# Kernel optimization log

Hardware: AMD Instinct MI355X
Metric: run time of the kernel (lower is better)

Reference implementation:

```python
import jax, jax.numpy as jnp
import numpy as np

N, F1, F2, D = 114, 32, 10, 100
F = F1 + F2
B = 16
EPS = 1e-5


def setup_inputs() -> dict:
    key = jax.random.key(0)
    ks = jax.random.split(key, 20)
    inp = {
        'XE_subs': jax.random.normal(ks[0], (B, 2, N, N, F), jnp.float32),
        'X_subs': jax.random.normal(ks[1], (B, 2, N, F1), jnp.float32),
        'A_subs': (jax.random.uniform(ks[2], (B, 2, N, N)) < 0.15).astype(jnp.float32),
        'XE_pros': jax.random.normal(ks[3], (B, 2, N, N, F), jnp.float32),
        'X_pros': jax.random.normal(ks[4], (B, 2, N, F1), jnp.float32),
        'A_pros': (jax.random.uniform(ks[5], (B, 2, N, N)) < 0.15).astype(jnp.float32),
        'Wi_sub': jax.random.normal(ks[6], (F, D)) * 0.1,
        'Wm1_sub': jax.random.normal(ks[7], (D, D)) * 0.1,
        'Wm2_sub': jax.random.normal(ks[8], (D, D)) * 0.1,
        'Wa_sub': jax.random.normal(ks[9], (D + F1, D)) * 0.1,
        'bn1s_g': jnp.ones((D,)), 'bn1s_b': jnp.zeros((D,)),
        'bn2s_g': jnp.ones((D,)), 'bn2s_b': jnp.zeros((D,)),
        'Wi_pro': jax.random.normal(ks[10], (F, D)) * 0.1,
        'Wm1_pro': jax.random.normal(ks[11], (D, D)) * 0.1,
        'Wm2_pro': jax.random.normal(ks[12], (D, D)) * 0.1,
        'Wa_pro': jax.random.normal(ks[13], (D + F1, D)) * 0.1,
        'bn1p_g': jnp.ones((D,)), 'bn1p_b': jnp.zeros((D,)),
        'bn2p_g': jnp.ones((D,)), 'bn2p_b': jnp.zeros((D,)),
        'bn3_g': jnp.ones((2 * D,)), 'bn3_b': jnp.zeros((2 * D,)),
        'W1': jax.random.normal(ks[14], (2 * D, 32)) * 0.07,
        'b1': jnp.zeros((32,)),
        'W2': jax.random.normal(ks[15], (32, 1)) * 0.17,
        'b2': jnp.zeros((1,)),
        'no_subs': 2, 'no_pros': 2,
    }
    return inp


def _bn4(x, g, b):
    # BatchNorm2d (training stats) over channel = last axis of [B,N,N,D]
    m = jnp.mean(x, axis=(0, 1, 2))
    v = jnp.var(x, axis=(0, 1, 2))
    return (x - m) * (g * jax.lax.rsqrt(v + EPS)) + b


def _branch(XE, X, A, no, Wi, Wm1, Wm2, Wa, g1, b1, g2, b2):
    h_max = None
    for i in range(no):
        xe = XE[:, i]                      # [B,N,N,F]
        a = A[:, i][..., None]             # [B,N,N,1]
        x = X[:, i][:, :, None, :]         # [B,N,1,F1]
        H0 = jax.nn.relu(jnp.einsum('bijf,fd->bijd', xe, Wi))  # [B,N,N,D]

        def mp(H):
            # Ones[N,N] @ transpose(H*A,1,2): column sum of (H*A) over axis 1,
            # broadcast, minus H^T, re-masked by A.
            S = jnp.sum(H * a, axis=1)                          # [B,N,D]
            return (S[:, :, None, :] - jnp.swapaxes(H, 1, 2)) * a

        H1 = jax.nn.relu(_bn4(H0 + jnp.einsum('bijd,de->bije', mp(H0), Wm1), g1, b1))
        H2 = jax.nn.relu(_bn4(H0 + jnp.einsum('bijd,de->bije', mp(H1), Wm2), g2, b2))
        Mv = jnp.sum(H2 * a, axis=2, keepdims=True)             # [B,N,1,D]
        XM = jnp.concatenate([x, Mv], axis=3)                   # [B,N,1,F1+D]
        H = jax.nn.relu(jnp.einsum('bnkf,fd->bnkd', XM, Wa))    # [B,N,1,D]
        h = jnp.sum(H[:, :, 0, :], axis=1)                      # [B,D]  (Ones1_N sum)
        h_max = h if h_max is None else jnp.maximum(h_max, h)
    return h_max


def reference(XE_subs, X_subs, A_subs, XE_pros, X_pros, A_pros,
              Wi_sub, Wm1_sub, Wm2_sub, Wa_sub, bn1s_g, bn1s_b, bn2s_g, bn2s_b,
              Wi_pro, Wm1_pro, Wm2_pro, Wa_pro, bn1p_g, bn1p_b, bn2p_g, bn2p_b,
              bn3_g, bn3_b, W1, b1, W2, b2, no_subs, no_pros):
    h_sub = _branch(XE_subs, X_subs, A_subs, int(no_subs),
                    Wi_sub, Wm1_sub, Wm2_sub, Wa_sub, bn1s_g, bn1s_b, bn2s_g, bn2s_b)
    h_pro = _branch(XE_pros, X_pros, A_pros, int(no_pros),
                    Wi_pro, Wm1_pro, Wm2_pro, Wa_pro, bn1p_g, bn1p_b, bn2p_g, bn2p_b)
    h = jnp.concatenate([h_sub, h_pro], axis=1)                 # [B,2D]
    m = jnp.mean(h, axis=0)
    v = jnp.var(h, axis=0)
    h = (h - m) * (bn3_g * jax.lax.rsqrt(v + EPS)) + bn3_b      # BatchNorm1d
    h = jax.nn.relu(h @ W1 + b1)
    return h @ W2 + b2                                          # [B,1]
```

## Files before the change

kernel.cpp:

```cpp
#include <hip/hip_runtime.h>

#define NN_ 114
#define NSQ (114*114)
#define FF 42
#define F1_ 32
#define DD 100
#define BB 16
#define ROWS (BB*NSQ)
#define NT512 407
#define MAXE 2432
#define NEB (MAXE/64)
#define MAXR 3968
#define EPS 1e-5f

typedef __attribute__((ext_vector_type(8))) short short8;
typedef __attribute__((ext_vector_type(4))) float f32x4;

static __device__ inline short f2bf(float f) {
    unsigned u;
    __builtin_memcpy(&u, &f, 4);
    unsigned r = (u + 0x7FFFu + ((u >> 16) & 1u)) >> 16;
    return (short)r;
}
static __device__ inline float bf2f(short h) {
    unsigned u = ((unsigned)(unsigned short)h) << 16;
    float f;
    __builtin_memcpy(&f, &u, 4);
    return f;
}

__global__ __launch_bounds__(1024) void k_edges(const float* __restrict__ Aa0,
                                                const float* __restrict__ Aa1,
                                                int* __restrict__ Eij, int* __restrict__ Idx,
                                                int* __restrict__ Ridx, int* __restrict__ Rlist,
                                                int* __restrict__ cnt, int* __restrict__ rcnt) {
    int b = blockIdx.x, combo = blockIdx.y;
    int zb = combo*BB + b;
    const float* am = ((combo < 2) ? Aa0 : Aa1) + (long)(b*2 + (combo & 1))*NSQ;
    int tid = threadIdx.x;
    __shared__ unsigned long long m0[NN_], m1[NN_];
    __shared__ int base_e, base_u;
    __shared__ int we[16], wu[16];
    int lane = tid & 63, wv = tid >> 6;
    if (tid == 0) { base_e = 0; base_u = 0; }
    for (int i = wv; i < NN_; i += 16) {
        float v0 = am[i*NN_ + lane];
        unsigned long long w0 = __ballot(v0 != 0.f);
        float v1 = (lane < NN_-64) ? am[i*NN_ + 64 + lane] : 0.f;
        unsigned long long w1 = __ballot(v1 != 0.f);
        if (lane == 0) { m0[i] = w0; m1[i] = w1; }
    }
    __syncthreads();
    for (int c0 = 0; c0 < NSQ; c0 += 1024) {
        int idx = c0 + tid;
        bool pe = false, pu = false;
        if (idx < NSQ) {
            int ii = idx / NN_, jj = idx - ii*NN_;
            pe = (((jj < 64 ? (m0[ii] >> jj) : (m1[ii] >> (jj-64))) & 1ull) != 0);
            bool pt = (((ii < 64 ? (m0[jj] >> ii) : (m1[jj] >> (ii-64))) & 1ull) != 0);
            pu = pe || pt;
        }
        unsigned long long me = __ballot(pe), mu = __ballot(pu);
        if (lane == 0) { we[wv] = __popcll(me); wu[wv] = __popcll(mu); }
        __syncthreads();
        int oe = base_e, ou = base_u;
        for (int w = 0; w < wv; w++) { oe += we[w]; ou += wu[w]; }
        oe += __popcll(me & ((1ull << lane) - 1ull));
        ou += __popcll(mu & ((1ull << lane) - 1ull));
        if (idx < NSQ) {
            bool oke = pe && (oe < MAXE);
            Idx[(long)zb*NSQ + idx]  = oke ? oe : -1;
            if (oke) Eij[zb*MAXE + oe] = idx;
            bool oku = pu && (ou < MAXR);
            Ridx[(long)zb*NSQ + idx] = oku ? ou : -1;
            if (oku) Rlist[(long)zb*MAXR + ou] = idx;
        }
        __syncthreads();
        if (tid == 0) { for (int w = 0; w < 16; w++) { base_e += we[w]; base_u += wu[w]; } }
        __syncthreads();
    }
    if (tid == 0) {
        cnt[zb]  = (base_e < MAXE) ? base_e : MAXE;
        rcnt[zb] = (base_u < MAXR) ? base_u : MAXR;
    }
}

__global__ __launch_bounds__(256) void k_h0stat(const float* __restrict__ XE0,
                                                const float* __restrict__ XE1,
                                                const float* __restrict__ Wi0,
                                                const float* __restrict__ Wi1,
                                                float* __restrict__ P0) {
    __shared__ char smem[16384 + 14336];
    char* Abase = smem;
    char* Bbase = smem + 16384;
    int tid = threadIdx.x;
    int combo = blockIdx.y;
    const float* XE = (combo < 2) ? XE0 : XE1;
    const float* Wi = (combo < 2) ? Wi0 : Wi1;
    int slot = combo & 1;
    for (int c = tid; c < 896; c += 256) {
        int col = c >> 3, k8b = (c & 7) * 8;
        short8 pk;
#pragma unroll
        for (int t = 0; t < 8; t++) {
            int k = k8b + t;
            pk[t] = (col < DD && k < FF) ? f2bf(Wi[k*DD + col]) : (short)0;
        }
        int byte = (col*128 + k8b*2) ^ ((col & 7) << 4);
        *reinterpret_cast<short8*>(Bbase + byte) = pk;
    }
    int w = tid >> 6, l = tid & 63;
    int lr = l & 15, g = l >> 4;
    float psum[7], psq[7];
#pragma unroll
    for (int ct = 0; ct < 7; ct++) { psum[ct] = 0.f; psq[ct] = 0.f; }
    int k8 = (tid & 7) * 8;
    int rbase = tid >> 3;
    for (int sub = 0; sub < 4; sub++) {
        int tileRow = blockIdx.x * 512 + sub * 128;
        float av[4][8];
#pragma unroll
        for (int c4 = 0; c4 < 4; c4++) {
            int r = tileRow + rbase + c4*32;
            if (r < ROWS && k8 < FF) {
                int b = r / NSQ;
                int ij = r - b*NSQ;
                const float* src = XE + ((long)(b*2 + slot)*NSQ + ij)*FF + k8;
                if (k8 <= 32) {
#pragma unroll
                    for (int q = 0; q < 4; q++) {
                        float2 f = *reinterpret_cast<const float2*>(src + q*2);
                        av[c4][q*2] = f.x; av[c4][q*2+1] = f.y;
                    }
                } else {
                    float2 f = *reinterpret_cast<const float2*>(src);
                    av[c4][0] = f.x; av[c4][1] = f.y;
#pragma unroll
                    for (int q = 2; q < 8; q++) av[c4][q] = 0.f;
                }
            } else {
#pragma unroll
                for (int q = 0; q < 8; q++) av[c4][q] = 0.f;
            }
        }
        __syncthreads();
#pragma unroll
        for (int c4 = 0; c4 < 4; c4++) {
            int row = rbase + c4*32;
            short8 pk;
#pragma unroll
            for (int t = 0; t < 8; t++) pk[t] = f2bf(av[c4][t]);
            int byte = (row*128 + k8*2) ^ ((row & 7) << 4);
            *reinterpret_cast<short8*>(Abase + byte) = pk;
        }
        __syncthreads();
        short8 af[2][2];
#pragma unroll
        for (int rt = 0; rt < 2; rt++) {
            int row = (w*2 + rt)*16 + lr;
#pragma unroll
            for (int kf = 0; kf < 2; kf++) {
                int byte = (row*128 + kf*64 + g*16) ^ ((row & 7) << 4);
                af[rt][kf] = *reinterpret_cast<const short8*>(Abase + byte);
            }
        }
#pragma unroll
        for (int ct = 0; ct < 7; ct++) {
            int col = ct*16 + lr;
            int bb0 = (col*128 +  0 + g*16) ^ ((col & 7) << 4);
            int bb1 = (col*128 + 64 + g*16) ^ ((col & 7) << 4);
            short8 bf0 = *reinterpret_cast<const short8*>(Bbase + bb0);
            short8 bf1 = *reinterpret_cast<const short8*>(Bbase + bb1);
            f32x4 a0 = (f32x4){0.f,0.f,0.f,0.f};
            f32x4 a1 = (f32x4){0.f,0.f,0.f,0.f};
            a0 = __builtin_amdgcn_mfma_f32_16x16x32_bf16(af[0][0], bf0, a0, 0, 0, 0);
            a0 = __builtin_amdgcn_mfma_f32_16x16x32_bf16(af[0][1], bf1, a0, 0, 0, 0);
            a1 = __builtin_amdgcn_mfma_f32_16x16x32_bf16(af[1][0], bf0, a1, 0, 0, 0);
            a1 = __builtin_amdgcn_mfma_f32_16x16x32_bf16(af[1][1], bf1, a1, 0, 0, 0);
#pragma unroll
            for (int rr = 0; rr < 4; rr++) {
                float v0 = fmaxf(a0[rr], 0.f);
                float v1 = fmaxf(a1[rr], 0.f);
                psum[ct] += v0 + v1;
                psq[ct]  += v0*v0 + v1*v1;
            }
        }
    }
    __syncthreads();
    float* red_s = (float*)smem;
    float* red_q = red_s + 16*112;
    int idx16 = w*4 + g;
#pragma unroll
    for (int ct = 0; ct < 7; ct++) {
        red_s[idx16*112 + ct*16 + lr] = psum[ct];
        red_q[idx16*112 + ct*16 + lr] = psq[ct];
    }
    __syncthreads();
    if (tid < DD) {
        float s = 0.f, q = 0.f;
#pragma unroll
        for (int t2 = 0; t2 < 16; t2++) { s += red_s[t2*112 + tid]; q += red_q[t2*112 + tid]; }
        P0[((long)combo*NT512 + blockIdx.x)*200 + tid] = s;
        P0[((long)combo*NT512 + blockIdx.x)*200 + 100 + tid] = q;
    }
}

__global__ __launch_bounds__(256) void k_h0u(const float* __restrict__ XE0,
                                             const float* __restrict__ XE1,
                                             const float* __restrict__ Wi0,
                                             const float* __restrict__ Wi1,
                                             const int* __restrict__ Rlist,
                                             const int* __restrict__ rcnt,
                                             float* __restrict__ H0c, int zbase) {
    __shared__ float smem[FF*68 + FF*112];
    float* As = smem;
    float* Bs = smem + FF*68;
    __shared__ int srcOff[64];
    int tid = threadIdx.x;
    int b = blockIdx.y, z = blockIdx.z;
    int combo = zbase + z;
    const float* XE = (combo < 2) ? XE0 : XE1;
    const float* Wi = (combo < 2) ? Wi0 : Wi1;
    int slot = combo & 1;
    int zbE = combo*BB + b;
    int zbH = z*BB + b;
    int rid0 = blockIdx.x * 64;
    int rc = rcnt[zbE];
    if (rid0 >= rc) return;
    if (tid < 64) {
        int rid = rid0 + tid;
        int ij = (rid < rc) ? Rlist[(long)zbE*MAXR + rid] : Rlist[(long)zbE*MAXR];
        srcOff[tid] = ((b*2+slot)*NSQ + ij)*FF;
    }
    for (int idx = tid; idx < FF*112; idx += 256) {
        int kk = idx / 112, col = idx - kk*112;
        Bs[idx] = (col < DD) ? Wi[kk*DD + col] : 0.f;
    }
    __syncthreads();
    for (int idx = tid; idx < 64*FF; idx += 256) {
        int rr = idx / FF, kk = idx - rr*FF;
        As[kk*68 + rr] = XE[(long)srcOff[rr] + kk];
    }
    int ty = tid >> 4, tx = tid & 15;
    float acc[4][7];
#pragma unroll
    for (int i = 0; i < 4; i++)
#pragma unroll
        for (int j = 0; j < 7; j++) acc[i][j] = 0.f;
    __syncthreads();
    for (int kk = 0; kk < FF; kk++) {
        float4 avv = *reinterpret_cast<const float4*>(&As[kk*68 + ty*4]);
#pragma unroll
        for (int cc = 0; cc < 7; cc++) {
            float bv = Bs[kk*112 + tx + 16*cc];
            acc[0][cc] += avv.x*bv; acc[1][cc] += avv.y*bv;
            acc[2][cc] += avv.z*bv; acc[3][cc] += avv.w*bv;
        }
    }
#pragma unroll
    for (int rq = 0; rq < 4; rq++) {
        int rid = rid0 + ty*4 + rq;
        if (rid < rc) {
#pragma unroll
            for (int cc = 0; cc < 7; cc++) {
                int col = tx + 16*cc;
                if (col < DD)
                    H0c[((long)zbH*MAXR + rid)*DD + col] = fmaxf(acc[rq][cc], 0.f);
            }
        }
    }
}

template<int LAYER>
__global__ __launch_bounds__(128) void k_cs(const float* __restrict__ H0c,
                                            const int* __restrict__ Idx,
                                            const int* __restrict__ Ridx,
                                            const float* __restrict__ Dprev,
                                            const float* __restrict__ bnsc,
                                            float* __restrict__ CSp, int zbase) {
    int bi = blockIdx.x, part = blockIdx.y, z = blockIdx.z;
    int b = bi / NN_, i = bi % NN_;
    int zbE = (zbase + z)*BB + b;
    int zbH = z*BB + b;
    int k0 = part*29, k1 = (k0+29 < NN_) ? k0+29 : NN_;
    __shared__ int eid_s[29], row_s[29];
    int tid = threadIdx.x;
    if (tid < k1-k0) {
        long pos = (long)zbE*NSQ + (k0+tid)*NN_ + i;
        eid_s[tid] = Idx[pos];
        row_s[tid] = Ridx[pos];
    }
    __syncthreads();
    if (tid < DD) {
        float sc = 0.f, sh = 0.f;
        if (LAYER == 2) { sc = bnsc[z*200 + tid]; sh = bnsc[z*200 + DD + tid]; }
        float acc = 0.f;
        for (int k = 0; k < k1-k0; k++) {
            int e = eid_s[k];
            if (e >= 0) {
                float v = H0c[((long)zbH*MAXR + row_s[k])*DD + tid];
                if (LAYER == 2) { v += Dprev[((long)zbH*MAXE + e)*DD + tid]; v = fmaxf(v*sc+sh, 0.f); }
                acc += v;
            }
        }
        CSp[(((long)z*BB*NN_ + bi)*4 + part)*DD + tid] = acc;
    }
}

__global__ __launch_bounds__(256) void k_swgemm(const float* __restrict__ CSp,
                                                const float* __restrict__ W0,
                                                const float* __restrict__ W1,
                                                float* __restrict__ SW, int zbase) {
    const int M = BB*NN_;
    __shared__ float smem[50*68 + 50*DD];
    float* As = smem;
    float* Bs = smem + 50*68;
    int tid = threadIdx.x;
    int z = blockIdx.y;
    const float* W = ((zbase + z) < 2) ? W0 : W1;
    const float* In = CSp + (long)z*M*4*DD;
    float* Out = SW + (long)z*M*DD;
    int tileRow = blockIdx.x * 64;
    int ty = tid >> 4, tx = tid & 15;
    float acc[4][7];
#pragma unroll
    for (int i=0;i<4;i++)
#pragma unroll
        for (int j=0;j<7;j++) acc[i][j]=0.f;
    for (int kc = 0; kc < 2; kc++) {
        __syncthreads();
        for (int idx = tid; idx < 64*50; idx += 256) {
            int rr = idx / 50, kk = idx % 50;
            int r = tileRow + rr;
            float v = 0.f;
            if (r < M) {
                long base = (long)r*4*DD + kc*50 + kk;
                v = In[base] + In[base+DD] + In[base+2*DD] + In[base+3*DD];
            }
            As[kk*68 + rr] = v;
        }
        for (int idx = tid; idx < 50*DD; idx += 256) {
            int kk = idx / DD, e = idx % DD;
            Bs[kk*DD + e] = W[(kc*50+kk)*DD + e];
        }
        __syncthreads();
        for (int kk = 0; kk < 50; kk++) {
            float4 av = *reinterpret_cast<const float4*>(&As[kk*68 + ty*4]);
#pragma unroll
            for (int cc=0; cc<7; cc++) {
                int col = tx + 16*cc;
                float bv = (col < DD) ? Bs[kk*DD + col] : 0.f;
                acc[0][cc] += av.x*bv; acc[1][cc] += av.y*bv;
                acc[2][cc] += av.z*bv; acc[3][cc] += av.w*bv;
            }
        }
    }
#pragma unroll
    for (int rq=0;rq<4;rq++){
        int r = tileRow + ty*4 + rq;
        if (r < M) {
#pragma unroll
            for (int cc=0;cc<7;cc++){
                int col = tx+16*cc;
                if (col < DD) Out[(long)r*DD + col] = acc[rq][cc];
            }
        }
    }
}

template<int LAYER>
__global__ __launch_bounds__(256) void k_dcomb(const float* __restrict__ H0c,
                                               const int* __restrict__ Eij,
                                               const int* __restrict__ cnt,
                                               const int* __restrict__ Idx,
                                               const int* __restrict__ Ridx,
                                               const float* __restrict__ Dprev,
                                               const float* __restrict__ Wm0,
                                               const float* __restrict__ Wm1,
                                               const float* __restrict__ SW,
                                               const float* __restrict__ bnsc,
                                               float* __restrict__ Dout,
                                               float* __restrict__ PD, int zbase) {
    __shared__ char smem[45056];
    char* Ahi = smem;
    char* Alo = smem + 8192;
    char* Bhi = smem + 16384;
    char* Blo = smem + 16384 + 14336;
    __shared__ int srcOff[64], addOff[64], h0Off[64], swOff[64];
    __shared__ float s1[DD], t1[DD];
    int tid = threadIdx.x;
    int b = blockIdx.y, z = blockIdx.z;
    int combo = zbase + z;
    const float* Wm = (combo < 2) ? Wm0 : Wm1;
    int zbE = combo*BB + b;
    int zbH = z*BB + b;
    int e0 = blockIdx.x * 64;
    int c = cnt[zbE];
    long pdbase = ((long)zbH*NEB + blockIdx.x)*200;
    if (e0 >= c) {
        if (tid < DD) { PD[pdbase + tid] = 0.f; PD[pdbase + 100 + tid] = 0.f; }
        return;
    }
    if (LAYER == 2 && tid < DD) { s1[tid]=bnsc[z*200+tid]; t1[tid]=bnsc[z*200+DD+tid]; }
    if (tid < 64) {
        int e = e0 + tid;
        if (e < c) {
            int ij = Eij[zbE*MAXE + e];
            int ii = ij / NN_, jj = ij % NN_;
            long tpos = (long)zbE*NSQ + jj*NN_ + ii;
            srcOff[tid] = (zbH*MAXR + Ridx[tpos])*DD;
            h0Off[tid]  = (zbH*MAXR + Ridx[(long)zbE*NSQ + ij])*DD;
            swOff[tid]  = ((z*BB + b)*NN_ + ii)*DD;
            if (LAYER == 2) {
                int et = Idx[tpos];
                addOff[tid] = (et >= 0) ? (zbH*MAXE + et)*DD : -1;
            } else addOff[tid] = -1;
        } else { srcOff[tid]=0; h0Off[tid]=0; swOff[tid]=0; addOff[tid]=-1; }
    }
    int w = tid >> 6, l = tid & 63;
    int lr = l & 15, g = l >> 4;
    f32x4 acc[7];
#pragma unroll
    for (int ct = 0; ct < 7; ct++) acc[ct] = (f32x4){0.f,0.f,0.f,0.f};
    for (int kc = 0; kc < 2; kc++) {
        __syncthreads();
        for (int idx = tid; idx < 512; idx += 256) {
            int row = idx >> 3, k8 = (idx & 7) * 8;
            int kbase = kc*64 + k8;
            const float* src = H0c + srcOff[row] + kbase;
            const float* dsrc = (LAYER == 2 && addOff[row] >= 0) ? (Dprev + addOff[row] + kbase) : nullptr;
            short8 hi, lo;
#pragma unroll
            for (int t = 0; t < 8; t++) {
                int k = kbase + t;
                float x = 0.f;
                if (k < DD) {
                    x = src[t];
                    if (LAYER == 2) {
                        if (dsrc) x += dsrc[t];
                        x = fmaxf(x*s1[k] + t1[k], 0.f);
                    }
                }
                short h = f2bf(x);
                hi[t] = h;
                lo[t] = f2bf(x - bf2f(h));
            }
            int byte = (row*128 + k8*2) ^ ((row & 7) << 4);
            *reinterpret_cast<short8*>(Ahi + byte) = hi;
            *reinterpret_cast<short8*>(Alo + byte) = lo;
        }
        for (int idx = tid; idx < 896; idx += 256) {
            int col = idx >> 3, k8 = (idx & 7) * 8;
            short8 hi, lo;
#pragma unroll
            for (int t = 0; t < 8; t++) {
                int k = kc*64 + k8 + t;
                float x = (col < DD && k < DD) ? Wm[k*DD + col] : 0.f;
                short h = f2bf(x);
                hi[t] = h;
                lo[t] = f2bf(x - bf2f(h));
            }
            int byte = (col*128 + k8*2) ^ ((col & 7) << 4);
            *reinterpret_cast<short8*>(Bhi + byte) = hi;
            *reinterpret_cast<short8*>(Blo + byte) = lo;
        }
        __syncthreads();
        int arow = w*16 + lr;
        short8 ah[2], al[2];
#pragma unroll
        for (int kf = 0; kf < 2; kf++) {
            int byte = (arow*128 + kf*64 + g*16) ^ ((arow & 7) << 4);
            ah[kf] = *reinterpret_cast<const short8*>(Ahi + byte);
            al[kf] = *reinterpret_cast<const short8*>(Alo + byte);
        }
#pragma unroll
        for (int ct = 0; ct < 7; ct++) {
            int col = ct*16 + lr;
#pragma unroll
            for (int kf = 0; kf < 2; kf++) {
                int byte = (col*128 + kf*64 + g*16) ^ ((col & 7) << 4);
                short8 bh = *reinterpret_cast<const short8*>(Bhi + byte);
                short8 bl = *reinterpret_cast<const short8*>(Blo + byte);
                acc[ct] = __builtin_amdgcn_mfma_f32_16x16x32_bf16(ah[kf], bh, acc[ct], 0, 0, 0);
                acc[ct] = __builtin_amdgcn_mfma_f32_16x16x32_bf16(ah[kf], bl, acc[ct], 0, 0, 0);
                acc[ct] = __builtin_amdgcn_mfma_f32_16x16x32_bf16(al[kf], bh, acc[ct], 0, 0, 0);
            }
        }
    }
    float psum[7], psq[7];
#pragma unroll
    for (int ct = 0; ct < 7; ct++) { psum[ct] = 0.f; psq[ct] = 0.f; }
#pragma unroll
    for (int reg = 0; reg < 4; reg++) {
        int rloc = w*16 + g*4 + reg;
        int e = e0 + rloc;
        if (e < c) {
            long doff = ((long)zbH*MAXE + e)*DD;
            int swo = swOff[rloc], h0o = h0Off[rloc];
#pragma unroll
            for (int ct = 0; ct < 7; ct++) {
                int col = ct*16 + lr;
                if (col < DD) {
                    float d = SW[swo + col] - acc[ct][reg];
                    Dout[doff + col] = d;
                    float hh = H0c[h0o + col];
                    psum[ct] += d;
                    psq[ct]  += (2.f*hh + d)*d;
                }
            }
        }
    }
    __syncthreads();
    float* red_s = (float*)smem;
    float* red_q = red_s + 16*112;
    int idx16 = w*4 + g;
#pragma unroll
    for (int ct = 0; ct < 7; ct++) {
        red_s[idx16*112 + ct*16 + lr] = psum[ct];
        red_q[idx16*112 + ct*16 + lr] = psq[ct];
    }
    __syncthreads();
    if (tid < DD) {
        float s = 0.f, q = 0.f;
#pragma unroll
        for (int t2 = 0; t2 < 16; t2++) { s += red_s[t2*112 + tid]; q += red_q[t2*112 + tid]; }
        PD[pdbase + tid] = s;
        PD[pdbase + 100 + tid] = q;
    }
}

__global__ __launch_bounds__(256) void k_bnfin(const float* __restrict__ P0,
                                               const float* __restrict__ PD,
                                               const float* __restrict__ g0,
                                               const float* __restrict__ g1,
                                               const float* __restrict__ bb0,
                                               const float* __restrict__ bb1,
                                               float* __restrict__ bnsc, int zbase) {
    __shared__ float rs[256], rq[256];
    int e = blockIdx.x, z = blockIdx.y;
    int combo = zbase + z;
    const float* g  = (combo < 2) ? g0  : g1;
    const float* bb = (combo < 2) ? bb0 : bb1;
    int tid = threadIdx.x;
    const float* P = PD + (long)z*BB*NEB*200;
    float s=0.f,q=0.f;
    for (int p=tid; p<BB*NEB; p+=256){ s += P[(long)p*200 + e]; q += P[(long)p*200 + 100 + e]; }
    const float* PP = P0 + (long)combo*NT512*200;
    for (int p=tid; p<NT512; p+=256){ s += PP[(long)p*200 + e]; q += PP[(long)p*200 + 100 + e]; }
    rs[tid]=s; rq[tid]=q; __syncthreads();
    for (int off=128; off>0; off>>=1){
        if (tid<off){ rs[tid]+=rs[tid+off]; rq[tid]+=rq[tid+off]; }
        __syncthreads();
    }
    if (tid==0){
        float m = rs[0]/(float)ROWS;
        float var = rq[0]/(float)ROWS - m*m;
        float sc = g[e]*rsqrtf(var+EPS);
        bnsc[z*200 + e] = sc;
        bnsc[z*200 + DD + e] = bb[e] - m*sc;
    }
}

__global__ __launch_bounds__(128) void k_mvxm(const float* __restrict__ H0c,
                                              const int* __restrict__ Idx,
                                              const int* __restrict__ Ridx,
                                              const float* __restrict__ D2,
                                              const float* __restrict__ bnsc,
                                              const float* __restrict__ X0,
                                              const float* __restrict__ X1,
                                              const float* __restrict__ Wa0,
                                              const float* __restrict__ Wa1,
                                              float* __restrict__ hpart, int zbase) {
    int n = blockIdx.x, b = blockIdx.y, z = blockIdx.z;
    int combo = zbase + z;
    const float* X  = (combo < 2) ? X0  : X1;
    const float* Wa = (combo < 2) ? Wa0 : Wa1;
    int slot = combo & 1;
    int zbE = combo*BB + b;
    int zbH = z*BB + b;
    int tid = threadIdx.x;
    __shared__ int eid_s[NN_], row_s[NN_];
    __shared__ float xm[132];
    if (tid < NN_) {
        long pos = (long)zbE*NSQ + n*NN_ + tid;
        eid_s[tid] = Idx[pos];
        row_s[tid] = Ridx[pos];
    }
    if (tid < F1_) xm[tid] = X[((long)(b*2+slot)*NN_ + n)*F1_ + tid];
    __syncthreads();
    if (tid < DD) {
        float sc = bnsc[z*200+tid], sh = bnsc[z*200+DD+tid];
        float acc = 0.f;
        for (int j = 0; j < NN_; j++) {
            int e = eid_s[j];
            if (e >= 0) {
                float v = H0c[((long)zbH*MAXR + row_s[j])*DD + tid]
                        + D2[((long)zbH*MAXE + e)*DD + tid];
                acc += fmaxf(v*sc + sh, 0.f);
            }
        }
        xm[F1_ + tid] = acc;
    }
    __syncthreads();
    if (tid < DD) {
        float acc = 0.f;
        for (int f = 0; f < 132; f++) acc += xm[f]*Wa[f*DD + tid];
        hpart[(((long)combo*BB + b)*NN_ + n)*DD + tid] = fmaxf(acc, 0.f);
    }
}

__global__ __launch_bounds__(128) void k_hred(const float* __restrict__ hpart,
                                              float* __restrict__ h) {
    int cb = blockIdx.x;
    int tid = threadIdx.x;
    if (tid < DD) {
        float acc = 0.f;
        for (int n = 0; n < NN_; n++) acc += hpart[((long)cb*NN_ + n)*DD + tid];
        h[(long)cb*DD + tid] = acc;
    }
}

__global__ __launch_bounds__(256) void k_head(const float* __restrict__ h,
                                              const float* __restrict__ g3, const float* __restrict__ b3,
                                              const float* __restrict__ W1, const float* __restrict__ b1,
                                              const float* __restrict__ W2, const float* __restrict__ b2,
                                              float* __restrict__ out) {
    __shared__ float hl[BB][200];
    __shared__ float z[BB][32];
    int tid = threadIdx.x;
    for (int idx=tid; idx<BB*200; idx+=256){
        int b = idx/200, c = idx%200;
        float v;
        if (c < DD) v = fmaxf(h[(0*BB+b)*DD + c],        h[(1*BB+b)*DD + c]);
        else        v = fmaxf(h[(2*BB+b)*DD + (c-DD)],   h[(3*BB+b)*DD + (c-DD)]);
        hl[b][c] = v;
    }
    __syncthreads();
    if (tid < 200){
        float m=0.f;
        for (int b=0;b<BB;b++) m += hl[b][tid];
        m *= (1.f/BB);
        float v=0.f;
        for (int b=0;b<BB;b++){ float d = hl[b][tid]-m; v += d*d; }
        v *= (1.f/BB);
        float sc = g3[tid]*rsqrtf(v+EPS);
        float sh = b3[tid] - m*sc;
        for (int b=0;b<BB;b++) hl[b][tid] = hl[b][tid]*sc + sh;
    }
    __syncthreads();
    for (int idx=tid; idx<BB*32; idx+=256){
        int b = idx/32, k = idx%32;
        float accv = b1[k];
        for (int c=0;c<200;c++) accv += hl[b][c]*W1[c*32+k];
        z[b][k] = fmaxf(accv, 0.f);
    }
    __syncthreads();
    if (tid < BB){
        float accv = b2[0];
        for (int k=0;k<32;k++) accv += z[tid][k]*W2[k];
        out[tid] = accv;
    }
}

extern "C" void kernel_launch(void* const* d_in, const int* in_sizes, int n_in,
                              void* d_out, int out_size, void* d_ws, size_t ws_size,
                              hipStream_t stream) {
    const float* XE[2]  = {(const float*)d_in[0],  (const float*)d_in[3]};
    const float* Xi[2]  = {(const float*)d_in[1],  (const float*)d_in[4]};
    const float* Aa[2]  = {(const float*)d_in[2],  (const float*)d_in[5]};
    const float* Wi[2]  = {(const float*)d_in[6],  (const float*)d_in[14]};
    const float* Wm1[2] = {(const float*)d_in[7],  (const float*)d_in[15]};
    const float* Wm2[2] = {(const float*)d_in[8],  (const float*)d_in[16]};
    const float* Wa[2]  = {(const float*)d_in[9],  (const float*)d_in[17]};
    const float* g1[2]  = {(const float*)d_in[10], (const float*)d_in[18]};
    const float* bb1[2] = {(const float*)d_in[11], (const float*)d_in[19]};
    const float* g2[2]  = {(const float*)d_in[12], (const float*)d_in[20]};
    const float* bb2[2] = {(const float*)d_in[13], (const float*)d_in[21]};

    const long perNC  = (long)BB*MAXR*DD + 2L*BB*MAXE*DD + (long)BB*NN_*4*DD
                      + (long)BB*NN_*DD + (long)BB*NEB*200;
    const long fixedF = 4L*NT512*200 + 2048 + 4L*BB*NN_*DD + 6400;
    const long intsN  = 4L*BB*MAXE + 8L*BB*NSQ + 4L*BB*MAXR + 128;
    int NC = (ws_size >= (size_t)(4L*perNC + fixedF + intsN) * 4) ? 4 : 2;

    float* p = (float*)d_ws;
    float* H0c = p;  p += (long)NC*BB*MAXR*DD;
    float* D1  = p;  p += (long)NC*BB*MAXE*DD;
    float* D2  = p;  p += (long)NC*BB*MAXE*DD;
    float* CSp = p;  p += (long)NC*BB*NN_*4*DD;
    float* SW  = p;  p += (long)NC*BB*NN_*DD;
    float* PD  = p;  p += (long)NC*BB*NEB*200;
    float* P0  = p;  p += 4L*NT512*200;
    float* bns1= p;  p += 1024;
    float* bns2= p;  p += 1024;
    float* hpart=p;  p += 4L*BB*NN_*DD;
    float* h   = p;  p += 6400;
    int* Eij   = (int*)p;
    int* Idx   = Eij  + 4*BB*MAXE;
    int* Ridx  = Idx  + 4*BB*NSQ;
    int* Rlist = Ridx + 4*BB*NSQ;
    int* cnt   = Rlist + 4*BB*MAXR;
    int* rcnt  = cnt + 64;

    k_edges<<<dim3(BB, 4), 1024, 0, stream>>>(Aa[0], Aa[1], Eij, Idx, Ridx, Rlist, cnt, rcnt);
    k_h0stat<<<dim3(NT512, 4), 256, 0, stream>>>(XE[0], XE[1], Wi[0], Wi[1], P0);

    for (int g = 0; g < 4; g += NC) {
        k_h0u<<<dim3(MAXR/64, BB, NC), 256, 0, stream>>>(XE[0], XE[1], Wi[0], Wi[1],
                                                         Rlist, rcnt, H0c, g);
        k_cs<1><<<dim3(BB*NN_, 4, NC), 128, 0, stream>>>(H0c, Idx, Ridx, nullptr, nullptr, CSp, g);
        k_swgemm<<<dim3(29, NC), 256, 0, stream>>>(CSp, Wm1[0], Wm1[1], SW, g);
        k_dcomb<1><<<dim3(NEB, BB, NC), 256, 0, stream>>>(H0c, Eij, cnt, Idx, Ridx, nullptr,
                                                          Wm1[0], Wm1[1], SW, nullptr, D1, PD, g);
        k_bnfin<<<dim3(DD, NC), 256, 0, stream>>>(P0, PD, g1[0], g1[1], bb1[0], bb1[1], bns1, g);
        k_cs<2><<<dim3(BB*NN_, 4, NC), 128, 0, stream>>>(H0c, Idx, Ridx, D1, bns1, CSp, g);
        k_swgemm<<<dim3(29, NC), 256, 0, stream>>>(CSp, Wm2[0], Wm2[1], SW, g);
        k_dcomb<2><<<dim3(NEB, BB, NC), 256, 0, stream>>>(H0c, Eij, cnt, Idx, Ridx, D1,
                                                          Wm2[0], Wm2[1], SW, bns1, D2, PD, g);
        k_bnfin<<<dim3(DD, NC), 256, 0, stream>>>(P0, PD, g2[0], g2[1], bb2[0], bb2[1], bns2, g);
        k_mvxm<<<dim3(NN_, BB, NC), 128, 0, stream>>>(H0c, Idx, Ridx, D2, bns2,
                                                      Xi[0], Xi[1], Wa[0], Wa[1], hpart, g);
    }
    k_hred<<<4*BB, 128, 0, stream>>>(hpart, h);
    k_head<<<1, 256, 0, stream>>>(h,
        (const float*)d_in[22], (const float*)d_in[23],
        (const float*)d_in[24], (const float*)d_in[25],
        (const float*)d_in[26], (const float*)d_in[27],
        (float*)d_out);
}
```

Before: 475.1 us.

## Pre-split Wm weights to bf16 hi/lo once and load MFMA operands directly

Adds a small kernel that converts the four Wm matrices into padded bf16 hi/lo arrays once per call. k_dcomb then reads its B fragments straight from global memory (L2-resident) and builds its A fragments in registers from vectorised float4 loads, instead of staging both through shared memory with repeated per-block conversion. This removes per-block weight conversion, the LDS round trip and the barriers. In exchange, each wave issues redundant global loads for the weight fragments and needs more workspace.

```diff
diff --git a/kernel.cpp b/kernel.cpp
--- a/kernel.cpp
+++ b/kernel.cpp
@@ -85,6 +85,24 @@
     }
 }
 
+__global__ __launch_bounds__(256) void k_wconv(const float* __restrict__ Wm10,
+                                               const float* __restrict__ Wm11,
+                                               const float* __restrict__ Wm20,
+                                               const float* __restrict__ Wm21,
+                                               short* __restrict__ Wmbf) {
+    int m = blockIdx.x;
+    const float* W = (m == 0) ? Wm10 : (m == 1) ? Wm11 : (m == 2) ? Wm20 : Wm21;
+    short* hi = Wmbf + (long)m*2*112*128;
+    short* lo = hi + 112*128;
+    for (int idx = threadIdx.x; idx < 112*128; idx += 256) {
+        int col = idx >> 7, k = idx & 127;
+        float x = (col < DD && k < DD) ? W[k*DD + col] : 0.f;
+        short h = f2bf(x);
+        hi[idx] = h;
+        lo[idx] = f2bf(x - bf2f(h));
+    }
+}
+
 __global__ __launch_bounds__(256) void k_h0stat(const float* __restrict__ XE0,
                                                 const float* __restrict__ XE1,
                                                 const float* __restrict__ Wi0,
@@ -375,23 +393,17 @@
                                                const int* __restrict__ Idx,
                                                const int* __restrict__ Ridx,
                                                const float* __restrict__ Dprev,
-                                               const float* __restrict__ Wm0,
-                                               const float* __restrict__ Wm1,
+                                               const short* __restrict__ WmbfL,
                                                const float* __restrict__ SW,
                                                const float* __restrict__ bnsc,
                                                float* __restrict__ Dout,
                                                float* __restrict__ PD, int zbase) {
-    __shared__ char smem[45056];
-    char* Ahi = smem;
-    char* Alo = smem + 8192;
-    char* Bhi = smem + 16384;
-    char* Blo = smem + 16384 + 14336;
     __shared__ int srcOff[64], addOff[64], h0Off[64], swOff[64];
     __shared__ float s1[DD], t1[DD];
+    __shared__ float red[2*16*112];
     int tid = threadIdx.x;
     int b = blockIdx.y, z = blockIdx.z;
     int combo = zbase + z;
-    const float* Wm = (combo < 2) ? Wm0 : Wm1;
     int zbE = combo*BB + b;
     int zbH = z*BB + b;
     int e0 = blockIdx.x * 64;
@@ -401,6 +413,8 @@
         if (tid < DD) { PD[pdbase + tid] = 0.f; PD[pdbase + 100 + tid] = 0.f; }
         return;
     }
+    const short* WBhi = WmbfL + (long)((combo < 2) ? 0 : 1)*2*112*128;
+    const short* WBlo = WBhi + 112*128;
     if (LAYER == 2 && tid < DD) { s1[tid]=bnsc[z*200+tid]; t1[tid]=bnsc[z*200+DD+tid]; }
     if (tid < 64) {
         int e = e0 + tid;
@@ -417,70 +431,70 @@
             } else addOff[tid] = -1;
         } else { srcOff[tid]=0; h0Off[tid]=0; swOff[tid]=0; addOff[tid]=-1; }
     }
+    __syncthreads();
     int w = tid >> 6, l = tid & 63;
     int lr = l & 15, g = l >> 4;
+    int arow = w*16 + lr;
+    int so = srcOff[arow];
+    int ao = (LAYER == 2) ? addOff[arow] : -1;
     f32x4 acc[7];
 #pragma unroll
     for (int ct = 0; ct < 7; ct++) acc[ct] = (f32x4){0.f,0.f,0.f,0.f};
+#pragma unroll
     for (int kc = 0; kc < 2; kc++) {
-        __syncthreads();
-        for (int idx = tid; idx < 512; idx += 256) {
-            int row = idx >> 3, k8 = (idx & 7) * 8;
-            int kbase = kc*64 + k8;
-            const float* src = H0c + srcOff[row] + kbase;
-            const float* dsrc = (LAYER == 2 && addOff[row] >= 0) ? (Dprev + addOff[row] + kbase) : nullptr;
-            short8 hi, lo;
+        short8 ah[2], al[2];
+#pragma unroll
+        for (int kf = 0; kf < 2; kf++) {
+            int kbase = kc*64 + kf*32 + g*8;
+            float x[8];
+            if (kbase + 8 <= DD) {
+                float4 f0 = *reinterpret_cast<const float4*>(H0c + so + kbase);
+                float4 f1 = *reinterpret_cast<const float4*>(H0c + so + kbase + 4);
+                x[0]=f0.x; x[1]=f0.y; x[2]=f0.z; x[3]=f0.w;
+                x[4]=f1.x; x[5]=f1.y; x[6]=f1.z; x[7]=f1.w;
+                if (LAYER == 2 && ao >= 0) {
+                    float4 d0 = *reinterpret_cast<const float4*>(Dprev + ao + kbase);
+                    float4 d1 = *reinterpret_cast<const float4*>(Dprev + ao + kbase + 4);
+                    x[0]+=d0.x; x[1]+=d0.y; x[2]+=d0.z; x[3]+=d0.w;
+                    x[4]+=d1.x; x[5]+=d1.y; x[6]+=d1.z; x[7]+=d1.w;
+                }
+            } else if (kbase < DD) {
+#pragma unroll
+                for (int t = 0; t < 8; t++) {
+                    int k = kbase + t;
+                    float v = 0.f;
+                    if (k < DD) {
+                        v = H0c[so + k];
+                        if (LAYER == 2 && ao >= 0) v += Dprev[ao + k];
+                    }
+                    x[t] = v;
+                }
+            } else {
+#pragma unroll
+                for (int t = 0; t < 8; t++) x[t] = 0.f;
+            }
+            if (LAYER == 2) {
+#pragma unroll
+                for (int t = 0; t < 8; t++) {
+                    int k = kbase + t;
+                    if (k < DD) x[t] = fmaxf(x[t]*s1[k] + t1[k], 0.f);
+                }
+            }
 #pragma unroll
             for (int t = 0; t < 8; t++) {
-                int k = kbase + t;
-                float x = 0.f;
-                if (k < DD) {
-                    x = src[t];
-                    if (LAYER == 2) {
-                        if (dsrc) x += dsrc[t];
-                        x = fmaxf(x*s1[k] + t1[k], 0.f);
-                    }
-                }
-                short h = f2bf(x);
-                hi[t] = h;
-                lo[t] = f2bf(x - bf2f(h));
-            }
-            int byte = (row*128 + k8*2) ^ ((row & 7) << 4);
-            *reinterpret_cast<short8*>(Ahi + byte) = hi;
-            *reinterpret_cast<short8*>(Alo + byte) = lo;
-        }
-        for (int idx = tid; idx < 896; idx += 256) {
-            int col = idx >> 3, k8 = (idx & 7) * 8;
-            short8 hi, lo;
-#pragma unroll
-            for (int t = 0; t < 8; t++) {
-                int k = kc*64 + k8 + t;
-                float x = (col < DD && k < DD) ? Wm[k*DD + col] : 0.f;
-                short h = f2bf(x);
-                hi[t] = h;
-                lo[t] = f2bf(x - bf2f(h));
-            }
-            int byte = (col*128 + k8*2) ^ ((col & 7) << 4);
-            *reinterpret_cast<short8*>(Bhi + byte) = hi;
-            *reinterpret_cast<short8*>(Blo + byte) = lo;
-        }
-        __syncthreads();
-        int arow = w*16 + lr;
-        short8 ah[2], al[2];
-#pragma unroll
-        for (int kf = 0; kf < 2; kf++) {
-            int byte = (arow*128 + kf*64 + g*16) ^ ((arow & 7) << 4);
-            ah[kf] = *reinterpret_cast<const short8*>(Ahi + byte);
-            al[kf] = *reinterpret_cast<const short8*>(Alo + byte);
+                short h = f2bf(x[t]);
+                ah[kf][t] = h;
+                al[kf][t] = f2bf(x[t] - bf2f(h));
+            }
         }
 #pragma unroll
         for (int ct = 0; ct < 7; ct++) {
             int col = ct*16 + lr;
 #pragma unroll
             for (int kf = 0; kf < 2; kf++) {
-                int byte = (col*128 + kf*64 + g*16) ^ ((col & 7) << 4);
-                short8 bh = *reinterpret_cast<const short8*>(Bhi + byte);
-                short8 bl = *reinterpret_cast<const short8*>(Blo + byte);
+                int koff = col*128 + kc*64 + kf*32 + g*8;
+                short8 bh = *reinterpret_cast<const short8*>(WBhi + koff);
+                short8 bl = *reinterpret_cast<const short8*>(WBlo + koff);
                 acc[ct] = __builtin_amdgcn_mfma_f32_16x16x32_bf16(ah[kf], bh, acc[ct], 0, 0, 0);
                 acc[ct] = __builtin_amdgcn_mfma_f32_16x16x32_bf16(ah[kf], bl, acc[ct], 0, 0, 0);
                 acc[ct] = __builtin_amdgcn_mfma_f32_16x16x32_bf16(al[kf], bh, acc[ct], 0, 0, 0);
@@ -510,9 +524,8 @@
             }
         }
     }
-    __syncthreads();
-    float* red_s = (float*)smem;
-    float* red_q = red_s + 16*112;
+    float* red_s = red;
+    float* red_q = red + 16*112;
     int idx16 = w*4 + g;
 #pragma unroll
     for (int ct = 0; ct < 7; ct++) {
@@ -679,7 +692,7 @@
 
     const long perNC  = (long)BB*MAXR*DD + 2L*BB*MAXE*DD + (long)BB*NN_*4*DD
                       + (long)BB*NN_*DD + (long)BB*NEB*200;
-    const long fixedF = 4L*NT512*200 + 2048 + 4L*BB*NN_*DD + 6400;
+    const long fixedF = 4L*NT512*200 + 2048 + 4L*BB*NN_*DD + 6400 + 57344;
     const long intsN  = 4L*BB*MAXE + 8L*BB*NSQ + 4L*BB*MAXR + 128;
     int NC = (ws_size >= (size_t)(4L*perNC + fixedF + intsN) * 4) ? 4 : 2;
 
@@ -695,6 +708,7 @@
     float* bns2= p;  p += 1024;
     float* hpart=p;  p += 4L*BB*NN_*DD;
     float* h   = p;  p += 6400;
+    short* Wmbf = (short*)p; p += 57344;
     int* Eij   = (int*)p;
     int* Idx   = Eij  + 4*BB*MAXE;
     int* Ridx  = Idx  + 4*BB*NSQ;
@@ -703,6 +717,7 @@
     int* rcnt  = cnt + 64;
 
     k_edges<<<dim3(BB, 4), 1024, 0, stream>>>(Aa[0], Aa[1], Eij, Idx, Ridx, Rlist, cnt, rcnt);
+    k_wconv<<<4, 256, 0, stream>>>(Wm1[0], Wm1[1], Wm2[0], Wm2[1], Wmbf);
     k_h0stat<<<dim3(NT512, 4), 256, 0, stream>>>(XE[0], XE[1], Wi[0], Wi[1], P0);
 
     for (int g = 0; g < 4; g += NC) {
@@ -711,12 +726,12 @@
         k_cs<1><<<dim3(BB*NN_, 4, NC), 128, 0, stream>>>(H0c, Idx, Ridx, nullptr, nullptr, CSp, g);
         k_swgemm<<<dim3(29, NC), 256, 0, stream>>>(CSp, Wm1[0], Wm1[1], SW, g);
         k_dcomb<1><<<dim3(NEB, BB, NC), 256, 0, stream>>>(H0c, Eij, cnt, Idx, Ridx, nullptr,
-                                                          Wm1[0], Wm1[1], SW, nullptr, D1, PD, g);
+                                                          Wmbf, SW, nullptr, D1, PD, g);
         k_bnfin<<<dim3(DD, NC), 256, 0, stream>>>(P0, PD, g1[0], g1[1], bb1[0], bb1[1], bns1, g);
         k_cs<2><<<dim3(BB*NN_, 4, NC), 128, 0, stream>>>(H0c, Idx, Ridx, D1, bns1, CSp, g);
         k_swgemm<<<dim3(29, NC), 256, 0, stream>>>(CSp, Wm2[0], Wm2[1], SW, g);
         k_dcomb<2><<<dim3(NEB, BB, NC), 256, 0, stream>>>(H0c, Eij, cnt, Idx, Ridx, D1,
-                                                          Wm2[0], Wm2[1], SW, bns1, D2, PD, g);
+                                                          Wmbf + 2L*2*112*128, SW, bns1, D2, PD, g);
         k_bnfin<<<dim3(DD, NC), 256, 0, stream>>>(P0, PD, g2[0], g2[1], bb2[0], bb2[1], bns2, g);
         k_mvxm<<<dim3(NN_, BB, NC), 128, 0, stream>>>(H0c, Idx, Ridx, D2, bns2,
                                                       Xi[0], Xi[1], Wa[0], Wa[1], hpart, g);
```

New measurement: 514.9 us. 1.08x slower.
